# Optimization experiments

Measured on AMD Instinct MI355X. Metric: run time of the kernel, lower is better.

Reference implementation:

```python
import jax, jax.numpy as jnp
import numpy as np


def setup_inputs() -> dict:
    key = jax.random.key(0)
    k1, k2, k3, k4 = jax.random.split(key, 4)
    B, P, K = 512, 1024, 64  # batch, n_points, n_components
    x = jax.random.normal(k1, (B, P), dtype=jnp.float32)
    # params init: uniform(-0.01, 0.01) as in reset_parameters
    a = jax.random.uniform(k2, (P, K, 1), dtype=jnp.float32, minval=-0.01, maxval=0.01)
    b = jax.random.uniform(k3, (P, K, 1), dtype=jnp.float32, minval=-0.01, maxval=0.01)
    a0 = jax.random.uniform(k4, (1,), dtype=jnp.float32, minval=-0.01, maxval=0.01)
    return {"x": x, "a": a, "b": b, "a0": a0}


def reference(x, a, b, a0):
    # x: [B, P]; a, b: [P, K, 1]; a0: [1]
    P = x.shape[-1]
    K = a.shape[1]
    two_pi_over_P = jnp.asarray(2.0 * np.pi / P, dtype=x.dtype)
    n = jnp.arange(K, dtype=x.dtype)                    # component indices 0..K-1
    pa = x @ a[..., 0]                                  # [B, K]  (x @ a[:, n] batched)
    pb = x @ b[..., 0]                                  # [B, K]
    phase = two_pi_over_P * x[..., None] * n            # [B, P, K]
    out = (a0 / (2 * P)) * jnp.ones_like(x)             # a0/(2*n_points) * ones_like(x)
    out = out + jnp.einsum('bk,bpk->bp', pa, jnp.cos(phase))
    out = out + jnp.einsum('bk,bpk->bp', pb, jnp.sin(phase))
    return out
```

## Files before the change

kernel.cpp:

```cpp
#include <hip/hip_runtime.h>


constexpr int PN = 1024;
constexpr int KN = 64;

__global__ __launch_bounds__(256) void k_partial(
    const float* __restrict__ x,
    const float* __restrict__ a,
    const float* __restrict__ bco,
    float* __restrict__ pw)
{
    __shared__ float xs[32][64];

    const int t = threadIdx.x;
    const int pc = blockIdx.x;
    const int bt = blockIdx.y;
    const int p0 = pc * 64;
    const int b0 = bt * 32;

    {
        const int c = t & 15, row = t >> 4;
        #pragma unroll
        for (int h = 0; h < 2; ++h) {
            const int r = row + 16 * h;
            const float4 v = *(const float4*)(x + (size_t)(b0 + r) * PN + p0 + 4 * c);
            xs[r][4 * c + 0] = v.x; xs[r][4 * c + 1] = v.y;
            xs[r][4 * c + 2] = v.z; xs[r][4 * c + 3] = v.w;
        }
    }
    __syncthreads();

    const int kg = t & 15;
    const int bg = t >> 4;
    float sa[2][4] = {{0.f}}, sb[2][4] = {{0.f}};
    #pragma unroll 4
    for (int i = 0; i < 64; ++i) {
        const int p = p0 + i;
        const float4 av = *(const float4*)(a   + (size_t)p * KN + 4 * kg);
        const float4 bv = *(const float4*)(bco + (size_t)p * KN + 4 * kg);
        #pragma unroll
        for (int r = 0; r < 2; ++r) {
            const float xv = xs[2 * bg + r][i];
            sa[r][0] = fmaf(xv, av.x, sa[r][0]);
            sa[r][1] = fmaf(xv, av.y, sa[r][1]);
            sa[r][2] = fmaf(xv, av.z, sa[r][2]);
            sa[r][3] = fmaf(xv, av.w, sa[r][3]);
            sb[r][0] = fmaf(xv, bv.x, sb[r][0]);
            sb[r][1] = fmaf(xv, bv.y, sb[r][1]);
            sb[r][2] = fmaf(xv, bv.z, sb[r][2]);
            sb[r][3] = fmaf(xv, bv.w, sb[r][3]);
        }
    }

    #pragma unroll
    for (int r = 0; r < 2; ++r) {
        float* dst = pw + (((size_t)(b0 + 2 * bg + r) * 16 + pc) * 128) + 8 * kg;
        #pragma unroll
        for (int j = 0; j < 4; ++j) {
            float2 v; v.x = sa[r][j]; v.y = sb[r][j];
            *(float2*)(dst + 2 * j) = v;
        }
    }
}

__global__ __launch_bounds__(256) void k_out(
    const float* __restrict__ x,
    const float* __restrict__ pw,
    const float* __restrict__ a0,
    float* __restrict__ out)
{
    __shared__ float spab[2 * KN];

    const int t = threadIdx.x;
    const int b = blockIdx.x;

    if (t < 128) {
        const float* src = pw + (size_t)b * (16 * 128) + t;
        float s = 0.f;
        #pragma unroll
        for (int pc = 0; pc < 16; ++pc) s += src[pc * 128];
        spab[t] = s;
    }
    __syncthreads();

    const float4 xv4 = ((const float4*)(x + (size_t)b * PN))[t];
    const float xv[4] = {xv4.x, xv4.y, xv4.z, xv4.w};
    const float c0 = a0[0] * (1.0f / (2.0f * (float)PN));
    const float tp = (float)(6.283185307179586 / (double)PN);

    float cm1[4], sm1[4], cm2[4], sm2[4], t2[4], acc[4];
    const float pa0 = spab[0];
    const float pa1 = spab[2];
    const float pb1 = spab[3];
    #pragma unroll
    for (int j = 0; j < 4; ++j) {
        const float th = tp * xv[j];
        float c1, s1;
        __sincosf(th, &s1, &c1);
        t2[j]  = c1 + c1;
        cm2[j] = 1.f; sm2[j] = 0.f;
        cm1[j] = c1;  sm1[j] = s1;
        acc[j] = fmaf(pa1, c1, fmaf(pb1, s1, c0 + pa0));
    }
    #pragma unroll 8
    for (int k = 2; k < KN; ++k) {
        const float2 pk = *(const float2*)&spab[2 * k];
        #pragma unroll
        for (int j = 0; j < 4; ++j) {
            const float ck = fmaf(t2[j], cm1[j], -cm2[j]);
            const float sk = fmaf(t2[j], sm1[j], -sm2[j]);
            acc[j] = fmaf(pk.x, ck, acc[j]);
            acc[j] = fmaf(pk.y, sk, acc[j]);
            cm2[j] = cm1[j]; cm1[j] = ck;
            sm2[j] = sm1[j]; sm1[j] = sk;
        }
    }
    float4 o; o.x = acc[0]; o.y = acc[1]; o.z = acc[2]; o.w = acc[3];
    ((float4*)(out + (size_t)b * PN))[t] = o;
}

extern "C" void kernel_launch(void* const* d_in, const int* in_sizes, int n_in,
                              void* d_out, int out_size, void* d_ws, size_t ws_size,
                              hipStream_t stream) {
    const float* x  = (const float*)d_in[0];
    const float* a  = (const float*)d_in[1];
    const float* b  = (const float*)d_in[2];
    const float* a0 = (const float*)d_in[3];
    float* out = (float*)d_out;
    float* pw  = (float*)d_ws;

    k_partial<<<dim3(16, 16), dim3(256), 0, stream>>>(x, a, b, pw);
    k_out<<<dim3(512), dim3(256), 0, stream>>>(x, pw, a0, out);
}
```

Measured before the change: 84.57 us.

## Fuse partial and output kernels into one cooperative kernel with grid sync

Merges the two launches into a single cooperative kernel of 256 blocks. Each block computes its partial projections, then a grid-wide sync, then handles two batch rows of the Chebyshev-recurrence output stage. The x tile in shared memory now uses vectorized float4 stores and reads with a padded row. This removes one kernel launch and the gap between kernels, but adds grid-sync overhead and gives the output stage half as many blocks, each doing twice the work.

```diff
diff --git a/kernel.cpp b/kernel.cpp
--- a/kernel.cpp
+++ b/kernel.cpp
@@ -1,122 +1,134 @@
 #include <hip/hip_runtime.h>
+#include <hip/hip_cooperative_groups.h>
+
+namespace cg = cooperative_groups;
 
 
 constexpr int PN = 1024;
 constexpr int KN = 64;
 
-__global__ __launch_bounds__(256) void k_partial(
+__global__ __launch_bounds__(256) void fourier_coop(
     const float* __restrict__ x,
     const float* __restrict__ a,
     const float* __restrict__ bco,
-    float* __restrict__ pw)
+    const float* __restrict__ a0,
+    float* __restrict__ pw,
+    float* __restrict__ out)
 {
-    __shared__ float xs[32][64];
+    __shared__ float xs[32][68];
+    __shared__ float spab[2][2 * KN];
 
     const int t = threadIdx.x;
-    const int pc = blockIdx.x;
-    const int bt = blockIdx.y;
-    const int p0 = pc * 64;
-    const int b0 = bt * 32;
+    const int bid = blockIdx.x;
 
     {
-        const int c = t & 15, row = t >> 4;
+        const int pc = bid & 15;
+        const int bt = bid >> 4;
+        const int p0 = pc * 64;
+        const int b0 = bt * 32;
+
+        {
+            const int c = t & 15, row = t >> 4;
+            #pragma unroll
+            for (int h = 0; h < 2; ++h) {
+                const int r = row + 16 * h;
+                const float4 v = *(const float4*)(x + (size_t)(b0 + r) * PN + p0 + 4 * c);
+                *(float4*)&xs[r][4 * c] = v;
+            }
+        }
+        __syncthreads();
+
+        const int kg = t & 15;
+        const int bg = t >> 4;
+        float sa[2][4] = {{0.f}}, sb[2][4] = {{0.f}};
+        #pragma unroll 2
+        for (int i4 = 0; i4 < 16; ++i4) {
+            float xl[2][4];
+            *(float4*)&xl[0][0] = *(const float4*)&xs[2 * bg + 0][4 * i4];
+            *(float4*)&xl[1][0] = *(const float4*)&xs[2 * bg + 1][4 * i4];
+            #pragma unroll
+            for (int q = 0; q < 4; ++q) {
+                const int p = p0 + 4 * i4 + q;
+                const float4 av = *(const float4*)(a   + (size_t)p * KN + 4 * kg);
+                const float4 bv = *(const float4*)(bco + (size_t)p * KN + 4 * kg);
+                #pragma unroll
+                for (int r = 0; r < 2; ++r) {
+                    const float xv = xl[r][q];
+                    sa[r][0] = fmaf(xv, av.x, sa[r][0]);
+                    sa[r][1] = fmaf(xv, av.y, sa[r][1]);
+                    sa[r][2] = fmaf(xv, av.z, sa[r][2]);
+                    sa[r][3] = fmaf(xv, av.w, sa[r][3]);
+                    sb[r][0] = fmaf(xv, bv.x, sb[r][0]);
+                    sb[r][1] = fmaf(xv, bv.y, sb[r][1]);
+                    sb[r][2] = fmaf(xv, bv.z, sb[r][2]);
+                    sb[r][3] = fmaf(xv, bv.w, sb[r][3]);
+                }
+            }
+        }
+
         #pragma unroll
-        for (int h = 0; h < 2; ++h) {
-            const int r = row + 16 * h;
-            const float4 v = *(const float4*)(x + (size_t)(b0 + r) * PN + p0 + 4 * c);
-            xs[r][4 * c + 0] = v.x; xs[r][4 * c + 1] = v.y;
-            xs[r][4 * c + 2] = v.z; xs[r][4 * c + 3] = v.w;
+        for (int r = 0; r < 2; ++r) {
+            float* dst = pw + (((size_t)(b0 + 2 * bg + r) * 16 + pc) * 128) + 8 * kg;
+            #pragma unroll
+            for (int j = 0; j < 4; ++j) {
+                float2 v; v.x = sa[r][j]; v.y = sb[r][j];
+                *(float2*)(dst + 2 * j) = v;
+            }
         }
+    }
+
+    cg::this_grid().sync();
+
+    {
+        const int row = t >> 7;
+        const int idx = t & 127;
+        const float* src = pw + (size_t)(2 * bid + row) * (16 * 128) + idx;
+        float s = 0.f;
+        #pragma unroll
+        for (int pc = 0; pc < 16; ++pc) s += src[pc * 128];
+        spab[row][idx] = s;
     }
     __syncthreads();
 
-    const int kg = t & 15;
-    const int bg = t >> 4;
-    float sa[2][4] = {{0.f}}, sb[2][4] = {{0.f}};
-    #pragma unroll 4
-    for (int i = 0; i < 64; ++i) {
-        const int p = p0 + i;
-        const float4 av = *(const float4*)(a   + (size_t)p * KN + 4 * kg);
-        const float4 bv = *(const float4*)(bco + (size_t)p * KN + 4 * kg);
-        #pragma unroll
-        for (int r = 0; r < 2; ++r) {
-            const float xv = xs[2 * bg + r][i];
-            sa[r][0] = fmaf(xv, av.x, sa[r][0]);
-            sa[r][1] = fmaf(xv, av.y, sa[r][1]);
-            sa[r][2] = fmaf(xv, av.z, sa[r][2]);
-            sa[r][3] = fmaf(xv, av.w, sa[r][3]);
-            sb[r][0] = fmaf(xv, bv.x, sb[r][0]);
-            sb[r][1] = fmaf(xv, bv.y, sb[r][1]);
-            sb[r][2] = fmaf(xv, bv.z, sb[r][2]);
-            sb[r][3] = fmaf(xv, bv.w, sb[r][3]);
-        }
-    }
+    const float c0 = a0[0] * (1.0f / (2.0f * (float)PN));
+    const float tp = (float)(6.283185307179586 / (double)PN);
 
     #pragma unroll
     for (int r = 0; r < 2; ++r) {
-        float* dst = pw + (((size_t)(b0 + 2 * bg + r) * 16 + pc) * 128) + 8 * kg;
+        const int b = 2 * bid + r;
+        const float4 xv4 = ((const float4*)(x + (size_t)b * PN))[t];
+        const float xv[4] = {xv4.x, xv4.y, xv4.z, xv4.w};
+
+        float cm1[4], sm1[4], cm2[4], sm2[4], t2[4], acc[4];
+        const float pa0 = spab[r][0];
+        const float pa1 = spab[r][2];
+        const float pb1 = spab[r][3];
         #pragma unroll
         for (int j = 0; j < 4; ++j) {
-            float2 v; v.x = sa[r][j]; v.y = sb[r][j];
-            *(float2*)(dst + 2 * j) = v;
+            const float th = tp * xv[j];
+            float c1, s1;
+            __sincosf(th, &s1, &c1);
+            t2[j]  = c1 + c1;
+            cm2[j] = 1.f; sm2[j] = 0.f;
+            cm1[j] = c1;  sm1[j] = s1;
+            acc[j] = fmaf(pa1, c1, fmaf(pb1, s1, c0 + pa0));
         }
+        #pragma unroll 8
+        for (int k = 2; k < KN; ++k) {
+            const float2 pk = *(const float2*)&spab[r][2 * k];
+            #pragma unroll
+            for (int j = 0; j < 4; ++j) {
+                const float ck = fmaf(t2[j], cm1[j], -cm2[j]);
+                const float sk = fmaf(t2[j], sm1[j], -sm2[j]);
+                acc[j] = fmaf(pk.x, ck, acc[j]);
+                acc[j] = fmaf(pk.y, sk, acc[j]);
+                cm2[j] = cm1[j]; cm1[j] = ck;
+                sm2[j] = sm1[j]; sm1[j] = sk;
+            }
+        }
+        float4 o; o.x = acc[0]; o.y = acc[1]; o.z = acc[2]; o.w = acc[3];
+        ((float4*)(out + (size_t)b * PN))[t] = o;
     }
-}
-
-__global__ __launch_bounds__(256) void k_out(
-    const float* __restrict__ x,
-    const float* __restrict__ pw,
-    const float* __restrict__ a0,
-    float* __restrict__ out)
-{
-    __shared__ float spab[2 * KN];
-
-    const int t = threadIdx.x;
-    const int b = blockIdx.x;
-
-    if (t < 128) {
-        const float* src = pw + (size_t)b * (16 * 128) + t;
-        float s = 0.f;
-        #pragma unroll
-        for (int pc = 0; pc < 16; ++pc) s += src[pc * 128];
-        spab[t] = s;
-    }
-    __syncthreads();
-
-    const float4 xv4 = ((const float4*)(x + (size_t)b * PN))[t];
-    const float xv[4] = {xv4.x, xv4.y, xv4.z, xv4.w};
-    const float c0 = a0[0] * (1.0f / (2.0f * (float)PN));
-    const float tp = (float)(6.283185307179586 / (double)PN);
-
-    float cm1[4], sm1[4], cm2[4], sm2[4], t2[4], acc[4];
-    const float pa0 = spab[0];
-    const float pa1 = spab[2];
-    const float pb1 = spab[3];
-    #pragma unroll
-    for (int j = 0; j < 4; ++j) {
-        const float th = tp * xv[j];
-        float c1, s1;
-        __sincosf(th, &s1, &c1);
-        t2[j]  = c1 + c1;
-        cm2[j] = 1.f; sm2[j] = 0.f;
-        cm1[j] = c1;  sm1[j] = s1;
-        acc[j] = fmaf(pa1, c1, fmaf(pb1, s1, c0 + pa0));
-    }
-    #pragma unroll 8
-    for (int k = 2; k < KN; ++k) {
-        const float2 pk = *(const float2*)&spab[2 * k];
-        #pragma unroll
-        for (int j = 0; j < 4; ++j) {
-            const float ck = fmaf(t2[j], cm1[j], -cm2[j]);
-            const float sk = fmaf(t2[j], sm1[j], -sm2[j]);
-            acc[j] = fmaf(pk.x, ck, acc[j]);
-            acc[j] = fmaf(pk.y, sk, acc[j]);
-            cm2[j] = cm1[j]; cm1[j] = ck;
-            sm2[j] = sm1[j]; sm1[j] = sk;
-        }
-    }
-    float4 o; o.x = acc[0]; o.y = acc[1]; o.z = acc[2]; o.w = acc[3];
-    ((float4*)(out + (size_t)b * PN))[t] = o;
 }
 
 extern "C" void kernel_launch(void* const* d_in, const int* in_sizes, int n_in,
@@ -129,6 +141,8 @@
     float* out = (float*)d_out;
     float* pw  = (float*)d_ws;
 
-    k_partial<<<dim3(16, 16), dim3(256), 0, stream>>>(x, a, b, pw);
-    k_out<<<dim3(512), dim3(256), 0, stream>>>(x, pw, a0, out);
+    void* kargs[] = {(void*)&x, (void*)&a, (void*)&b, (void*)&a0,
+                     (void*)&pw, (void*)&out};
+    hipLaunchCooperativeKernel(fourier_coop, dim3(256), dim3(256),
+                               kargs, 0, stream);
 }
```

Result: slower. 119.1 us (+40.8%).
